# Kernel tuning notes

Hardware: AMD Instinct MI355X
Metric: run time of the kernel (lower is better)

Reference implementation:

```python
import jax, jax.numpy as jnp
import numpy as np

N = 8192   # samples
D = 128    # number of variables / towers (dims[0])
D1 = 128   # hidden width (dims[1])


def setup_inputs() -> dict:
    key = jax.random.key(0)
    k_x, k_w0, k_w1, k_b1 = jax.random.split(key, 4)
    x = jax.random.normal(k_x, (N, D), dtype=jnp.float32)
    # Layer 0: one Linear(D -> D1) per tower -> batched weight [D_towers, D1, D_in]
    W0 = jax.random.normal(k_w0, (D, D1, D), dtype=jnp.float32) * (1.0 / np.sqrt(D))
    # NOTEARS init: zero self-edge column i of tower i, zero layer-0 biases
    idx = jnp.arange(D)
    W0 = W0.at[idx, :, idx].set(0.0)
    b0 = jnp.zeros((D, D1), dtype=jnp.float32)
    # Layer 1: Linear(D1 -> 1) per tower
    W1 = jax.random.normal(k_w1, (D, 1, D1), dtype=jnp.float32) * (1.0 / np.sqrt(D1))
    b1 = jax.random.normal(k_b1, (D, 1), dtype=jnp.float32) * 0.05
    return {"x": x, "W0": W0, "b0": b0, "W1": W1, "b1": b1}


def reference(x, W0, b0, W1, b1):
    # binary-input check from the original forward
    binary = jnp.all((x == 0) | (x == 1))
    # Layer 0 for all D towers at once: [n,d] x [k,h,d] -> [n,k,h]
    h = jax.nn.sigmoid(jnp.einsum('nd,khd->nkh', x, W0) + b0)
    # Layer 1 (output dim 1 per tower): [n,k,h] x [k,h] -> [n,k]
    out = jnp.einsum('nkh,kh->nk', h, W1[:, 0, :]) + b1[:, 0]
    out = jnp.where(binary, jax.nn.sigmoid(out), out)
    return out
```

## Files before the change

kernel.cpp:

```cpp
#include <hip/hip_runtime.h>
#include <hip/hip_bf16.h>
#include <stdint.h>

#define N_SAMP 8192
#define D_TOW  128
#define D_HID  128

typedef __bf16 bf16x8 __attribute__((ext_vector_type(8)));
typedef float  f32x4  __attribute__((ext_vector_type(4)));

__device__ __forceinline__ ushort f2bf(float f) {
  union { float f; uint32_t u; } c; c.f = f;
  uint32_t u = c.u;
  return (ushort)((u + 0x7FFFu + ((u >> 16) & 1u)) >> 16);
}

__device__ __forceinline__ float fast_sigmoid(float p) {
  float e = __builtin_amdgcn_exp2f(p * -1.442695040888963f);
  return __builtin_amdgcn_rcpf(1.0f + e);
}

__global__ __launch_bounds__(256) void prep_kernel(
    const float* __restrict__ x, const float* __restrict__ w0,
    ushort* __restrict__ xb, ushort* __restrict__ w0b,
    int* __restrict__ flagArr) {
  const int NX4 = (N_SAMP * D_TOW) / 4;
  int bid = blockIdx.x;
  int tid = threadIdx.x;
  int t = bid * 256 + tid;
  if (bid < 1024) {
    __shared__ int sbad;
    if (tid == 0) sbad = 0;
    float4 v = ((const float4*)x)[t];
    bool bad = !(((v.x == 0.f) || (v.x == 1.f)) &&
                 ((v.y == 0.f) || (v.y == 1.f)) &&
                 ((v.z == 0.f) || (v.z == 1.f)) &&
                 ((v.w == 0.f) || (v.w == 1.f)));
    ushort4 o;
    o.x = f2bf(v.x); o.y = f2bf(v.y); o.z = f2bf(v.z); o.w = f2bf(v.w);
    ((ushort4*)xb)[t] = o;
    __syncthreads();
    if (__ballot(bad) != 0ull && (tid & 63) == 0) sbad = 1;
    __syncthreads();
    if (tid == 0) flagArr[bid] = sbad;
  } else {
    const float c = -1.442695040888963f;
    int j = t - NX4;
    float4 v = ((const float4*)w0)[j];
    ushort4 o;
    o.x = f2bf(c * v.x); o.y = f2bf(c * v.y);
    o.z = f2bf(c * v.z); o.w = f2bf(c * v.w);
    ((ushort4*)w0b)[j] = o;
  }
}

__device__ __forceinline__ void g2l16(const void* g, void* l) {
  __builtin_amdgcn_global_load_lds(
      (const __attribute__((address_space(1))) void*)g,
      (__attribute__((address_space(3))) void*)l, 16, 0, 0);
}

__global__ __launch_bounds__(256, 4) void towers_kernel(
    const ushort* __restrict__ xb, const ushort* __restrict__ w0b,
    const float* __restrict__ b0, const float* __restrict__ w1,
    const float* __restrict__ b1, const int* __restrict__ flagArr,
    float* __restrict__ out) {
  __shared__ __align__(16) ushort sX[128 * 64];
  __shared__ __align__(16) ushort sW[128 * 64];
  __shared__ float sRed[128][2];
  __shared__ int sBadW[4];

  int bid = blockIdx.x;
  int xcd = bid & 7;
  int idx = bid >> 3;
  int k  = xcd * 16 + (idx & 15);
  int n0 = (idx >> 4) * 128;

  int tid = threadIdx.x;
  int lane = tid & 63;
  int wave = tid >> 6;
  int q = lane >> 4;
  int cl = lane & 15;

  const ushort* xg = xb + n0 * 128;
  const ushort* wg = w0b + k * (128 * 128);

  int4 fv = ((const int4*)flagArr)[tid];
  int anyb = fv.x | fv.y | fv.z | fv.w;
  unsigned long long mb = __ballot(anyb != 0);
  if (lane == 0) sBadW[wave] = (mb != 0ull) ? 1 : 0;

  int R  = (wave >> 1) * 64;
  int Ch = (wave & 1) * 64;

  f32x4 acc[4][4];
#pragma unroll
  for (int hf = 0; hf < 4; ++hf)
#pragma unroll
    for (int nf = 0; nf < 4; ++nf)
      acc[hf][nf] = (f32x4){0.f, 0.f, 0.f, 0.f};

  int aBase[4], bBase[4];
#pragma unroll
  for (int f = 0; f < 4; ++f) {
    aBase[f] = (Ch + f * 16 + cl) * 128;
    bBase[f] = (R + f * 16 + cl) * 128;
  }

  int rowl = lane >> 3;
  int slot = lane & 7;

#pragma unroll
  for (int kb = 0; kb < 2; ++kb) {
#pragma unroll
    for (int i = 0; i < 4; ++i) {
      int row = wave * 32 + i * 8 + rowl;
      int c = slot ^ (row & 7);
      int goff = row * 128 + kb * 64 + c * 8;
      int lbase = (wave * 32 + i * 8) * 128;
      g2l16(xg + goff, (char*)sX + lbase);
      g2l16(wg + goff, (char*)sW + lbase);
    }
    __syncthreads();

#pragma unroll
    for (int t = 0; t < 2; ++t) {
      int ch = ((t * 4 + q) ^ (cl & 7)) << 4;
      bf16x8 a[4], b[4];
#pragma unroll
      for (int hf = 0; hf < 4; ++hf)
        a[hf] = *(const bf16x8*)((const char*)sW + aBase[hf] + ch);
#pragma unroll
      for (int nf = 0; nf < 4; ++nf)
        b[nf] = *(const bf16x8*)((const char*)sX + bBase[nf] + ch);
#pragma unroll
      for (int hf = 0; hf < 4; ++hf)
#pragma unroll
        for (int nf = 0; nf < 4; ++nf)
          acc[hf][nf] = __builtin_amdgcn_mfma_f32_16x16x32_bf16(
              a[hf], b[nf], acc[hf][nf], 0, 0, 0);
    }
    if (kb == 0) __syncthreads();
  }

  f32x4 bbs[4], wv[4];
#pragma unroll
  for (int hf = 0; hf < 4; ++hf) {
    int h = k * 128 + Ch + hf * 16 + q * 4;
    f32x4 b0v = *(const f32x4*)&b0[h];
    wv[hf] = *(const f32x4*)&w1[h];
    bbs[hf] = b0v * -1.442695040888963f;
  }
  float s[4] = {0.f, 0.f, 0.f, 0.f};
#pragma unroll
  for (int hf = 0; hf < 4; ++hf)
#pragma unroll
    for (int nf = 0; nf < 4; ++nf) {
      f32x4 qv = acc[hf][nf] + bbs[hf];
      float d0 = 1.0f + __builtin_amdgcn_exp2f(qv[0]);
      float d1 = 1.0f + __builtin_amdgcn_exp2f(qv[1]);
      float d2 = 1.0f + __builtin_amdgcn_exp2f(qv[2]);
      float d3 = 1.0f + __builtin_amdgcn_exp2f(qv[3]);
      float r01 = __builtin_amdgcn_rcpf(d0 * d1);
      float r23 = __builtin_amdgcn_rcpf(d2 * d3);
      s[nf] += wv[hf][0] * (r01 * d1);
      s[nf] += wv[hf][1] * (r01 * d0);
      s[nf] += wv[hf][2] * (r23 * d3);
      s[nf] += wv[hf][3] * (r23 * d2);
    }

#pragma unroll
  for (int m = 16; m <= 32; m <<= 1)
#pragma unroll
    for (int nf = 0; nf < 4; ++nf)
      s[nf] += __shfl_xor(s[nf], m, 64);

  if (q == 0) {
#pragma unroll
    for (int nf = 0; nf < 4; ++nf)
      sRed[R + nf * 16 + cl][wave & 1] = s[nf];
  }
  __syncthreads();

  if (tid < 128) {
    int anyBad = sBadW[0] | sBadW[1] | sBadW[2] | sBadW[3];
    float v = sRed[tid][0] + sRed[tid][1] + b1[k];
    if (anyBad == 0) v = fast_sigmoid(v);
    out[(size_t)(n0 + tid) * D_TOW + k] = v;
  }
}

extern "C" void kernel_launch(void* const* d_in, const int* in_sizes, int n_in,
                              void* d_out, int out_size, void* d_ws, size_t ws_size,
                              hipStream_t stream) {
  const float* x  = (const float*)d_in[0];
  const float* w0 = (const float*)d_in[1];
  const float* b0 = (const float*)d_in[2];
  const float* w1 = (const float*)d_in[3];
  const float* b1 = (const float*)d_in[4];
  float* out = (float*)d_out;

  char* ws = (char*)d_ws;
  int* flagArr = (int*)ws;
  ushort* xb  = (ushort*)(ws + 4096);
  ushort* w0b = (ushort*)(ws + 4096 + N_SAMP * D_TOW * 2);

  int total4 = (N_SAMP * D_TOW + D_TOW * D_HID * D_TOW) / 4;
  prep_kernel<<<total4 / 256, 256, 0, stream>>>(x, w0, xb, w0b, flagArr);

  towers_kernel<<<8192, 256, 0, stream>>>(xb, w0b, b0, w1, b1, flagArr, out);
}
```

Baseline: 129.1 us.

## Hoist tile loads, fold bias into accumulators, use packed math and larger prep blocks

The prep kernel now uses 1024-thread blocks, so only 256 flag entries are produced and the towers kernel reads one flag per thread. In the towers kernel the first K-half tile load is issued before the flag ballot and bias setup, so those overlap with it. The layer-0 bias is folded into the accumulator initial value, MFMA sections are wrapped in s_setprio, and the sigmoid-weighted reduction uses two-wide float vectors so it can map to packed FP32 instructions. These several small changes aim to trim prologue latency and epilogue ALU work, at the cost of larger prep blocks that may lower occupancy.

```diff
diff --git a/kernel.cpp b/kernel.cpp
--- a/kernel.cpp
+++ b/kernel.cpp
@@ -8,6 +8,7 @@
 
 typedef __bf16 bf16x8 __attribute__((ext_vector_type(8)));
 typedef float  f32x4  __attribute__((ext_vector_type(4)));
+typedef float  f32x2  __attribute__((ext_vector_type(2)));
 
 __device__ __forceinline__ ushort f2bf(float f) {
   union { float f; uint32_t u; } c; c.f = f;
@@ -20,15 +21,15 @@
   return __builtin_amdgcn_rcpf(1.0f + e);
 }
 
-__global__ __launch_bounds__(256) void prep_kernel(
+__global__ __launch_bounds__(1024) void prep_kernel(
     const float* __restrict__ x, const float* __restrict__ w0,
     ushort* __restrict__ xb, ushort* __restrict__ w0b,
     int* __restrict__ flagArr) {
   const int NX4 = (N_SAMP * D_TOW) / 4;
   int bid = blockIdx.x;
   int tid = threadIdx.x;
-  int t = bid * 256 + tid;
-  if (bid < 1024) {
+  int t = bid * 1024 + tid;
+  if (bid < 256) {
     __shared__ int sbad;
     if (tid == 0) sbad = 0;
     float4 v = ((const float4*)x)[t];
@@ -85,20 +86,35 @@
   const ushort* xg = xb + n0 * 128;
   const ushort* wg = w0b + k * (128 * 128);
 
-  int4 fv = ((const int4*)flagArr)[tid];
-  int anyb = fv.x | fv.y | fv.z | fv.w;
+  int R  = (wave >> 1) * 64;
+  int Ch = (wave & 1) * 64;
+
+  int rowl = lane >> 3;
+  int slot = lane & 7;
+
+#pragma unroll
+  for (int i = 0; i < 4; ++i) {
+    int row = wave * 32 + i * 8 + rowl;
+    int c = slot ^ (row & 7);
+    int goff = row * 128 + c * 8;
+    int lbase = (wave * 32 + i * 8) * 128;
+    g2l16(xg + goff, (char*)sX + lbase);
+    g2l16(wg + goff, (char*)sW + lbase);
+  }
+
+  int anyb = flagArr[tid];
   unsigned long long mb = __ballot(anyb != 0);
   if (lane == 0) sBadW[wave] = (mb != 0ull) ? 1 : 0;
 
-  int R  = (wave >> 1) * 64;
-  int Ch = (wave & 1) * 64;
-
   f32x4 acc[4][4];
 #pragma unroll
-  for (int hf = 0; hf < 4; ++hf)
+  for (int hf = 0; hf < 4; ++hf) {
+    int h = k * 128 + Ch + hf * 16 + q * 4;
+    f32x4 bbs = *(const f32x4*)&b0[h] * -1.442695040888963f;
 #pragma unroll
     for (int nf = 0; nf < 4; ++nf)
-      acc[hf][nf] = (f32x4){0.f, 0.f, 0.f, 0.f};
+      acc[hf][nf] = bbs;
+  }
 
   int aBase[4], bBase[4];
 #pragma unroll
@@ -107,20 +123,8 @@
     bBase[f] = (R + f * 16 + cl) * 128;
   }
 
-  int rowl = lane >> 3;
-  int slot = lane & 7;
-
 #pragma unroll
   for (int kb = 0; kb < 2; ++kb) {
-#pragma unroll
-    for (int i = 0; i < 4; ++i) {
-      int row = wave * 32 + i * 8 + rowl;
-      int c = slot ^ (row & 7);
-      int goff = row * 128 + kb * 64 + c * 8;
-      int lbase = (wave * 32 + i * 8) * 128;
-      g2l16(xg + goff, (char*)sX + lbase);
-      g2l16(wg + goff, (char*)sW + lbase);
-    }
     __syncthreads();
 
 #pragma unroll
@@ -133,41 +137,56 @@
 #pragma unroll
       for (int nf = 0; nf < 4; ++nf)
         b[nf] = *(const bf16x8*)((const char*)sX + bBase[nf] + ch);
+      __builtin_amdgcn_s_setprio(1);
 #pragma unroll
       for (int hf = 0; hf < 4; ++hf)
 #pragma unroll
         for (int nf = 0; nf < 4; ++nf)
           acc[hf][nf] = __builtin_amdgcn_mfma_f32_16x16x32_bf16(
               a[hf], b[nf], acc[hf][nf], 0, 0, 0);
+      __builtin_amdgcn_s_setprio(0);
     }
-    if (kb == 0) __syncthreads();
-  }
-
-  f32x4 bbs[4], wv[4];
+
+    if (kb == 0) {
+      __syncthreads();
+#pragma unroll
+      for (int i = 0; i < 4; ++i) {
+        int row = wave * 32 + i * 8 + rowl;
+        int c = slot ^ (row & 7);
+        int goff = row * 128 + 64 + c * 8;
+        int lbase = (wave * 32 + i * 8) * 128;
+        g2l16(xg + goff, (char*)sX + lbase);
+        g2l16(wg + goff, (char*)sW + lbase);
+      }
+    }
+  }
+
+  f32x2 s2[4] = {{0.f, 0.f}, {0.f, 0.f}, {0.f, 0.f}, {0.f, 0.f}};
 #pragma unroll
   for (int hf = 0; hf < 4; ++hf) {
     int h = k * 128 + Ch + hf * 16 + q * 4;
-    f32x4 b0v = *(const f32x4*)&b0[h];
-    wv[hf] = *(const f32x4*)&w1[h];
-    bbs[hf] = b0v * -1.442695040888963f;
-  }
-  float s[4] = {0.f, 0.f, 0.f, 0.f};
-#pragma unroll
-  for (int hf = 0; hf < 4; ++hf)
+    f32x4 wv = *(const f32x4*)&w1[h];
+    f32x2 wa = {wv[0], wv[1]};
+    f32x2 wb = {wv[2], wv[3]};
 #pragma unroll
     for (int nf = 0; nf < 4; ++nf) {
-      f32x4 qv = acc[hf][nf] + bbs[hf];
-      float d0 = 1.0f + __builtin_amdgcn_exp2f(qv[0]);
-      float d1 = 1.0f + __builtin_amdgcn_exp2f(qv[1]);
-      float d2 = 1.0f + __builtin_amdgcn_exp2f(qv[2]);
-      float d3 = 1.0f + __builtin_amdgcn_exp2f(qv[3]);
-      float r01 = __builtin_amdgcn_rcpf(d0 * d1);
-      float r23 = __builtin_amdgcn_rcpf(d2 * d3);
-      s[nf] += wv[hf][0] * (r01 * d1);
-      s[nf] += wv[hf][1] * (r01 * d0);
-      s[nf] += wv[hf][2] * (r23 * d3);
-      s[nf] += wv[hf][3] * (r23 * d2);
+      f32x4 qv = acc[hf][nf];
+      f32x2 dA = {1.0f + __builtin_amdgcn_exp2f(qv[0]),
+                  1.0f + __builtin_amdgcn_exp2f(qv[1])};
+      f32x2 dB = {1.0f + __builtin_amdgcn_exp2f(qv[2]),
+                  1.0f + __builtin_amdgcn_exp2f(qv[3])};
+      float rA = __builtin_amdgcn_rcpf(dA[0] * dA[1]);
+      float rB = __builtin_amdgcn_rcpf(dB[0] * dB[1]);
+      f32x2 cA = (f32x2){dA[1], dA[0]} * (f32x2){rA, rA};
+      f32x2 cB = (f32x2){dB[1], dB[0]} * (f32x2){rB, rB};
+      s2[nf] += wa * cA;
+      s2[nf] += wb * cB;
     }
+  }
+  float s[4];
+#pragma unroll
+  for (int nf = 0; nf < 4; ++nf)
+    s[nf] = s2[nf][0] + s2[nf][1];
 
 #pragma unroll
   for (int m = 16; m <= 32; m <<= 1)
@@ -205,8 +224,8 @@
   ushort* xb  = (ushort*)(ws + 4096);
   ushort* w0b = (ushort*)(ws + 4096 + N_SAMP * D_TOW * 2);
 
-  int total4 = (N_SAMP * D_TOW + D_TOW * D_HID * D_TOW) / 4;
-  prep_kernel<<<total4 / 256, 256, 0, stream>>>(x, w0, xb, w0b, flagArr);
+  int total = (N_SAMP * D_TOW + D_TOW * D_HID * D_TOW) / 4;
+  prep_kernel<<<total / 1024, 1024, 0, stream>>>(x, w0, xb, w0b, flagArr);
 
   towers_kernel<<<8192, 256, 0, stream>>>(xb, w0b, b0, w1, b1, flagArr, out);
 }
```

Result: faster. 119.9 us (-7.2%).
